# Kernel tuning notes

Hardware: AMD Instinct MI355X
Metric: run time of the kernel (lower is better)

The kernel has to match this reference:

```python
import jax, jax.numpy as jnp
import numpy as np

N = 100000
E = 3200000
IN_DIM = 256
HID = 128
OUT_DIM = 64


def setup_inputs() -> dict:
    key = jax.random.key(0)
    ks = jax.random.split(key, 8)
    features = jax.random.normal(ks[0], (N, IN_DIM), dtype=jnp.float32)
    edge_row = jax.random.randint(ks[1], (E,), 0, N, dtype=jnp.int32)
    edge_col = jax.random.randint(ks[2], (E,), 0, N, dtype=jnp.int32)
    edge_val = jax.random.uniform(ks[3], (E,), dtype=jnp.float32)
    W1 = jax.random.normal(ks[4], (IN_DIM, HID), dtype=jnp.float32) * (1.0 / np.sqrt(IN_DIM))
    b1 = jnp.zeros((HID,), dtype=jnp.float32)
    W2 = jax.random.normal(ks[5], (HID, OUT_DIM), dtype=jnp.float32) * (1.0 / np.sqrt(HID))
    b2 = jnp.zeros((OUT_DIM,), dtype=jnp.float32)
    return {"features": features, "edge_row": edge_row, "edge_col": edge_col,
            "edge_val": edge_val, "W1": W1, "b1": b1, "W2": W2, "b2": b2}


def reference(features, edge_row, edge_col, edge_val, W1, b1, W2, b2):
    # fc1: [N, IN_DIM] @ [IN_DIM, HID] + b1
    h = features @ W1 + b1                                   # [N, HID]
    # spmm(A, h): for each edge (r, c, v): out[r] += v * h[c]
    msgs = edge_val[:, None] * h[edge_col]                    # [E, HID] gather
    h = jax.ops.segment_sum(msgs, edge_row, num_segments=N)   # [N, HID] scatter-add
    h = jax.nn.relu(h)
    h = h @ W2 + b2                                           # [N, OUT_DIM]
    return jax.nn.log_softmax(h, axis=1)
```

## Files before the change

### kernel.cpp

```cpp
#include <hip/hip_runtime.h>
#include <math.h>

constexpr int IN_DIM  = 256;
constexpr int HID     = 128;
constexpr int OUT_DIM = 64;

constexpr int BROWS   = 128;
constexpr int NBUCK   = 782;
constexpr int CAP     = 4608;
constexpr int CAP2    = 5504;
constexpr int CHUNK2  = 2048;
constexpr int GC_STRIDE = 16;

typedef short  bf16x8 __attribute__((ext_vector_type(8)));
typedef float  f32x4  __attribute__((ext_vector_type(4)));
typedef float  f32x2  __attribute__((ext_vector_type(2)));
typedef int    i32x4  __attribute__((ext_vector_type(4)));

__device__ __forceinline__ unsigned short f2bf(float x) {
    union { float f; unsigned u; } v; v.f = x;
    unsigned r = v.u + 0x7FFF + ((v.u >> 16) & 1);
    return (unsigned short)(r >> 16);
}

__global__ __launch_bounds__(256) void wt_kernel(const float* __restrict__ W1,
                                                 const float* __restrict__ W2,
                                                 unsigned short* __restrict__ W1T,
                                                 unsigned short* __restrict__ W2T)
{
    int idx = blockIdx.x * 256 + threadIdx.x;
    if (idx < IN_DIM * HID) {
        int k = idx >> 7;
        int n = idx & 127;
        W1T[n * IN_DIM + k] = f2bf(W1[idx]);
    } else {
        int j = idx - IN_DIM * HID;
        int k = j >> 6;
        int n = j & 63;
        W2T[n * HID + k] = f2bf(W2[j]);
    }
}

__global__ __launch_bounds__(256) void fc1_bin_fused(
        const float* __restrict__ feat,
        const unsigned short* __restrict__ W1T,
        const float* __restrict__ b1,
        unsigned short* __restrict__ h1b, int N,
        const int* __restrict__ erow,
        const int* __restrict__ ecol,
        const float* __restrict__ eval,
        int* __restrict__ gCursor,
        int2* __restrict__ binned, int E)
{
    __shared__ int sCnt[NBUCK];
    __shared__ int sBase[NBUCK];

    const int nfc1 = (N + 63) >> 6;
    const int nbin = (E + CHUNK2 - 1) / CHUNK2;
    const int nInter = 2 * min(nfc1, nbin);
    const int b = blockIdx.x;

    bool isBin;
    int  id;
    if (b < nInter) { isBin = (b & 1); id = b >> 1; }
    else            { isBin = (nbin > nfc1); id = min(nfc1, nbin) + (b - nInter); }

    const int t = threadIdx.x;

    if (!isBin) {
        const int lane = t & 63;
        const int w    = t >> 6;
        const int quad = lane >> 4;
        const int ln15 = lane & 15;
        const int row0 = id * 64;

        int arow = row0 + w * 16 + ln15;
        if (arow >= N) arow = N - 1;
        const float* aptr = feat + (size_t)arow * IN_DIM + quad * 8;

        f32x4 acc[8];
#pragma unroll
        for (int i = 0; i < 8; ++i) acc[i] = (f32x4){0.f, 0.f, 0.f, 0.f};

#pragma unroll
        for (int ks = 0; ks < 8; ++ks) {
            float4 a0 = *(const float4*)(aptr + ks * 32);
            float4 a1 = *(const float4*)(aptr + ks * 32 + 4);
            bf16x8 afrag;
            afrag[0] = (short)f2bf(a0.x); afrag[1] = (short)f2bf(a0.y);
            afrag[2] = (short)f2bf(a0.z); afrag[3] = (short)f2bf(a0.w);
            afrag[4] = (short)f2bf(a1.x); afrag[5] = (short)f2bf(a1.y);
            afrag[6] = (short)f2bf(a1.z); afrag[7] = (short)f2bf(a1.w);
#pragma unroll
            for (int nt = 0; nt < 8; ++nt) {
                bf16x8 bfrag = *(const bf16x8*)&W1T[(size_t)(nt * 16 + ln15) * IN_DIM + ks * 32 + quad * 8];
                acc[nt] = __builtin_amdgcn_mfma_f32_16x16x32_bf16(afrag, bfrag, acc[nt], 0, 0, 0);
            }
        }

#pragma unroll
        for (int nt = 0; nt < 8; ++nt) {
            int col = nt * 16 + ln15;
            float bias = b1[col];
#pragma unroll
            for (int r = 0; r < 4; ++r) {
                int grow = row0 + w * 16 + quad * 4 + r;
                if (grow < N)
                    h1b[(size_t)grow * HID + col] = f2bf(acc[nt][r] + bias);
            }
        }
    } else {
        const int e0   = id * CHUNK2;
        const int eEnd = min(e0 + CHUNK2, E);

        for (int i = t; i < NBUCK; i += 256) sCnt[i] = 0;
        __syncthreads();

        for (int e = e0 + t; e < eEnd; e += 256)
            atomicAdd(&sCnt[erow[e] >> 7], 1);
        __syncthreads();

        for (int i = t; i < NBUCK; i += 256) {
            int c = sCnt[i];
            sBase[i] = c ? atomicAdd(&gCursor[i * GC_STRIDE], c) : 0;
            sCnt[i] = 0;
        }
        __syncthreads();

        for (int e = e0 + t; e < eEnd; e += 256) {
            int   r = erow[e];
            int   c = ecol[e];
            float v = eval[e];
            int   bk = r >> 7;
            int off = sBase[bk] + atomicAdd(&sCnt[bk], 1);
            if (off < CAP)
                binned[(size_t)bk * CAP + off] = make_int2((c << 8) | ((r & 127) << 25),
                                                           __float_as_int(v));
        }
    }
}

__global__ __launch_bounds__(256) void sort_bucket4(const int* __restrict__ gCursor,
                                                    const int2* __restrict__ binned,
                                                    int2* __restrict__ edges2,
                                                    int2* __restrict__ rowIdx, int N)
{
    __shared__ int2 sE[CAP];
    __shared__ int sHist[BROWS];
    __shared__ int sStart[BROWS + 1];
    __shared__ int sCur[BROWS];
    const int t  = threadIdx.x;
    const int b  = blockIdx.x;
    const int nE = min(gCursor[b * GC_STRIDE], CAP);
    const size_t baseIn  = (size_t)b * CAP;
    const size_t baseOut = (size_t)b * CAP2;

    if (t < BROWS) sHist[t] = 0;
    __syncthreads();

    for (int i = t; i < nE; i += 256) {
        int2 p = binned[baseIn + i];
        sE[i] = p;
        atomicAdd(&sHist[(unsigned)p.x >> 25], 1);
    }
    __syncthreads();

    if (t < BROWS) sStart[t + 1] = (sHist[t] + 7) & ~7;
    if (t == 0) sStart[0] = 0;
    __syncthreads();
    for (int o = 1; o < BROWS; o <<= 1) {
        int v = 0;
        if (t < BROWS) {
            v = sStart[t + 1];
            if (t >= o) v += sStart[t + 1 - o];
        }
        __syncthreads();
        if (t < BROWS) sStart[t + 1] = v;
        __syncthreads();
    }
    if (t < BROWS) sCur[t] = sStart[t];
    __syncthreads();

    for (int i = t; i < nE; i += 256) {
        int2 p = sE[i];
        int rl = (unsigned)p.x >> 25;
        int pos = atomicAdd(&sCur[rl], 1);
        edges2[baseOut + pos] = p;
    }

    if (t < BROWS) {
        int h  = sHist[t];
        int ph = (h + 7) & ~7;
        size_t p0 = baseOut + sStart[t];
        for (int k = h; k < ph; ++k)
            edges2[p0 + k] = make_int2(0, 0);
        int rr = b * BROWS + t;
        if (rr < N)
            rowIdx[rr] = make_int2((int)p0, (int)(p0 + ph));
    }
}

__global__ __launch_bounds__(256) void spmm_kernel(const int2* __restrict__ rowIdx,
                                                   const int2* __restrict__ edges2,
                                                   const unsigned short* __restrict__ h1b,
                                                   unsigned* __restrict__ h2b, int N)
{
    const int lane  = threadIdx.x & 63;
    const int lane4 = lane * 4;
    const int r     = (blockIdx.x * blockDim.x + threadIdx.x) >> 6;
    if (r >= N) return;
    const char* h1base = (const char*)h1b;

    const int2 se = rowIdx[r];
    int j = se.x;
    const int jend = se.y;
    f32x2 acc = (f32x2){0.f, 0.f};

    for (; j + 16 <= jend; j += 16) {
        i32x4 q[8];
#pragma unroll
        for (int u = 0; u < 8; ++u)
            q[u] = __builtin_nontemporal_load((const i32x4*)&edges2[j + u * 2]);
        unsigned g[16];
#pragma unroll
        for (int u = 0; u < 8; ++u) {
            g[2 * u]     = *(const unsigned*)(h1base + (q[u].x & 0x01FFFFFF) + lane4);
            g[2 * u + 1] = *(const unsigned*)(h1base + (q[u].z & 0x01FFFFFF) + lane4);
        }
#pragma unroll
        for (int u = 0; u < 8; ++u) {
            f32x2 h0 = (f32x2){__uint_as_float(g[2 * u] << 16),
                               __uint_as_float(g[2 * u] & 0xFFFF0000u)};
            f32x2 h1 = (f32x2){__uint_as_float(g[2 * u + 1] << 16),
                               __uint_as_float(g[2 * u + 1] & 0xFFFF0000u)};
            acc += h0 * __int_as_float(q[u].y);
            acc += h1 * __int_as_float(q[u].w);
        }
    }
    if (j < jend) {
        i32x4 q[4];
#pragma unroll
        for (int u = 0; u < 4; ++u)
            q[u] = __builtin_nontemporal_load((const i32x4*)&edges2[j + u * 2]);
        unsigned g[8];
#pragma unroll
        for (int u = 0; u < 4; ++u) {
            g[2 * u]     = *(const unsigned*)(h1base + (q[u].x & 0x01FFFFFF) + lane4);
            g[2 * u + 1] = *(const unsigned*)(h1base + (q[u].z & 0x01FFFFFF) + lane4);
        }
#pragma unroll
        for (int u = 0; u < 4; ++u) {
            f32x2 h0 = (f32x2){__uint_as_float(g[2 * u] << 16),
                               __uint_as_float(g[2 * u] & 0xFFFF0000u)};
            f32x2 h1 = (f32x2){__uint_as_float(g[2 * u + 1] << 16),
                               __uint_as_float(g[2 * u + 1] & 0xFFFF0000u)};
            acc += h0 * __int_as_float(q[u].y);
            acc += h1 * __int_as_float(q[u].w);
        }
    }

    float ax = fmaxf(acc.x, 0.f), ay = fmaxf(acc.y, 0.f);
    h2b[(size_t)r * 64 + lane] = (unsigned)f2bf(ax) | ((unsigned)f2bf(ay) << 16);
}

__global__ __launch_bounds__(256) void fc2_mfma(const unsigned short* __restrict__ h2b,
                                                const unsigned short* __restrict__ W2T,
                                                const float* __restrict__ b2,
                                                float* __restrict__ out, int N)
{
    const int t    = threadIdx.x;
    const int lane = t & 63;
    const int w    = t >> 6;
    const int quad = lane >> 4;
    const int ln15 = lane & 15;
    const int row0 = blockIdx.x * 64;

    int arow = row0 + w * 16 + ln15;
    if (arow >= N) arow = N - 1;

    f32x4 acc[4];
#pragma unroll
    for (int i = 0; i < 4; ++i) acc[i] = (f32x4){0.f, 0.f, 0.f, 0.f};

#pragma unroll
    for (int ks = 0; ks < 4; ++ks) {
        bf16x8 afrag = *(const bf16x8*)&h2b[(size_t)arow * HID + ks * 32 + quad * 8];
#pragma unroll
        for (int nt = 0; nt < 4; ++nt) {
            bf16x8 bfrag = *(const bf16x8*)&W2T[(size_t)(nt * 16 + ln15) * HID + ks * 32 + quad * 8];
            acc[nt] = __builtin_amdgcn_mfma_f32_16x16x32_bf16(afrag, bfrag, acc[nt], 0, 0, 0);
        }
    }

    float bias[4];
#pragma unroll
    for (int nt = 0; nt < 4; ++nt) bias[nt] = b2[nt * 16 + ln15];

#pragma unroll
    for (int r = 0; r < 4; ++r) {
        float v[4];
#pragma unroll
        for (int nt = 0; nt < 4; ++nt) v[nt] = acc[nt][r] + bias[nt];

        float m = fmaxf(fmaxf(v[0], v[1]), fmaxf(v[2], v[3]));
#pragma unroll
        for (int o = 1; o < 16; o <<= 1) m = fmaxf(m, __shfl_xor(m, o));
        float s = __expf(v[0] - m) + __expf(v[1] - m) +
                  __expf(v[2] - m) + __expf(v[3] - m);
#pragma unroll
        for (int o = 1; o < 16; o <<= 1) s += __shfl_xor(s, o);
        float ls = __logf(s);

        int grow = row0 + w * 16 + quad * 4 + r;
        if (grow < N) {
#pragma unroll
            for (int nt = 0; nt < 4; ++nt)
                out[(size_t)grow * OUT_DIM + nt * 16 + ln15] = v[nt] - m - ls;
        }
    }
}

extern "C" void kernel_launch(void* const* d_in, const int* in_sizes, int n_in,
                              void* d_out, int out_size, void* d_ws, size_t ws_size,
                              hipStream_t stream) {
    const float* feat = (const float*)d_in[0];
    const int*   erow = (const int*)d_in[1];
    const int*   ecol = (const int*)d_in[2];
    const float* eval = (const float*)d_in[3];
    const float* W1   = (const float*)d_in[4];
    const float* b1   = (const float*)d_in[5];
    const float* W2   = (const float*)d_in[6];
    const float* b2   = (const float*)d_in[7];
    float*       out  = (float*)d_out;

    const int N = in_sizes[0] / IN_DIM;
    const int E = in_sizes[1];

    unsigned short* h1b    = (unsigned short*)d_ws;
    unsigned short* h2b    = h1b + (size_t)N * HID;
    int2*           binned = (int2*)(h2b + (size_t)N * HID);
    int2*           edges2 = binned + (size_t)NBUCK * CAP;
    int2*           rowIdx = edges2 + (size_t)NBUCK * CAP2;
    unsigned short* W1T    = (unsigned short*)(rowIdx + N);
    unsigned short* W2T    = W1T + IN_DIM * HID;
    int*            gCursor= (int*)(W2T + HID * OUT_DIM);

    hipMemsetAsync(gCursor, 0, NBUCK * GC_STRIDE * sizeof(int), stream);

    wt_kernel<<<(IN_DIM * HID + HID * OUT_DIM) / 256, 256, 0, stream>>>(W1, W2, W1T, W2T);

    const int nfc1 = (N + 63) / 64;
    const int nbin = (E + CHUNK2 - 1) / CHUNK2;
    fc1_bin_fused<<<nfc1 + nbin, 256, 0, stream>>>(feat, W1T, b1, h1b, N,
                                                   erow, ecol, eval,
                                                   gCursor, binned, E);

    sort_bucket4<<<NBUCK, 256, 0, stream>>>(gCursor, binned, edges2, rowIdx, N);

    const int nblk = (N + 3) / 4;
    spmm_kernel<<<nblk, 256, 0, stream>>>(rowIdx, edges2, h1b,
                                          (unsigned*)h2b, N);
    fc2_mfma<<<(N + 63) / 64, 256, 0, stream>>>(h2b, W2T, b2, out, N);
}
```

Baseline: 477.7 us.

## Fuse SpMM and fc2/log-softmax into one kernel using LDS-staged fp32 W2

Merges the SpMM kernel and the MFMA fc2 kernel into a single 512-thread kernel. Each wave aggregates one row, applies ReLU and writes it to LDS. It then computes the 64 fc2 outputs with scalar FMAs against W2, which each block copies into LDS as fp32, and finishes with the log-softmax via wave shuffles. This removes the bf16 h2 intermediate write and read and one kernel launch, and drops the W2 transpose. In exchange, every block reloads the 32KB W2 from cache, needs about 36KB of LDS, waits on a barrier before starting its gathers, and replaces the MFMA matmul with plain FMAs.

```diff
diff --git a/kernel.cpp b/kernel.cpp
--- a/kernel.cpp
+++ b/kernel.cpp
@@ -24,21 +24,12 @@
 }
 
 __global__ __launch_bounds__(256) void wt_kernel(const float* __restrict__ W1,
-                                                 const float* __restrict__ W2,
-                                                 unsigned short* __restrict__ W1T,
-                                                 unsigned short* __restrict__ W2T)
+                                                 unsigned short* __restrict__ W1T)
 {
     int idx = blockIdx.x * 256 + threadIdx.x;
-    if (idx < IN_DIM * HID) {
-        int k = idx >> 7;
-        int n = idx & 127;
-        W1T[n * IN_DIM + k] = f2bf(W1[idx]);
-    } else {
-        int j = idx - IN_DIM * HID;
-        int k = j >> 6;
-        int n = j & 63;
-        W2T[n * HID + k] = f2bf(W2[j]);
-    }
+    int k = idx >> 7;
+    int n = idx & 127;
+    W1T[n * IN_DIM + k] = f2bf(W1[idx]);
 }
 
 __global__ __launch_bounds__(256) void fc1_bin_fused(
@@ -200,123 +191,102 @@
     }
 }
 
-__global__ __launch_bounds__(256) void spmm_kernel(const int2* __restrict__ rowIdx,
-                                                   const int2* __restrict__ edges2,
-                                                   const unsigned short* __restrict__ h1b,
-                                                   unsigned* __restrict__ h2b, int N)
-{
-    const int lane  = threadIdx.x & 63;
-    const int lane4 = lane * 4;
-    const int r     = (blockIdx.x * blockDim.x + threadIdx.x) >> 6;
-    if (r >= N) return;
-    const char* h1base = (const char*)h1b;
-
-    const int2 se = rowIdx[r];
-    int j = se.x;
-    const int jend = se.y;
-    f32x2 acc = (f32x2){0.f, 0.f};
-
-    for (; j + 16 <= jend; j += 16) {
-        i32x4 q[8];
-#pragma unroll
-        for (int u = 0; u < 8; ++u)
-            q[u] = __builtin_nontemporal_load((const i32x4*)&edges2[j + u * 2]);
-        unsigned g[16];
-#pragma unroll
-        for (int u = 0; u < 8; ++u) {
-            g[2 * u]     = *(const unsigned*)(h1base + (q[u].x & 0x01FFFFFF) + lane4);
-            g[2 * u + 1] = *(const unsigned*)(h1base + (q[u].z & 0x01FFFFFF) + lane4);
-        }
-#pragma unroll
-        for (int u = 0; u < 8; ++u) {
-            f32x2 h0 = (f32x2){__uint_as_float(g[2 * u] << 16),
-                               __uint_as_float(g[2 * u] & 0xFFFF0000u)};
-            f32x2 h1 = (f32x2){__uint_as_float(g[2 * u + 1] << 16),
-                               __uint_as_float(g[2 * u + 1] & 0xFFFF0000u)};
-            acc += h0 * __int_as_float(q[u].y);
-            acc += h1 * __int_as_float(q[u].w);
-        }
-    }
-    if (j < jend) {
-        i32x4 q[4];
-#pragma unroll
-        for (int u = 0; u < 4; ++u)
-            q[u] = __builtin_nontemporal_load((const i32x4*)&edges2[j + u * 2]);
-        unsigned g[8];
-#pragma unroll
-        for (int u = 0; u < 4; ++u) {
-            g[2 * u]     = *(const unsigned*)(h1base + (q[u].x & 0x01FFFFFF) + lane4);
-            g[2 * u + 1] = *(const unsigned*)(h1base + (q[u].z & 0x01FFFFFF) + lane4);
-        }
-#pragma unroll
-        for (int u = 0; u < 4; ++u) {
-            f32x2 h0 = (f32x2){__uint_as_float(g[2 * u] << 16),
-                               __uint_as_float(g[2 * u] & 0xFFFF0000u)};
-            f32x2 h1 = (f32x2){__uint_as_float(g[2 * u + 1] << 16),
-                               __uint_as_float(g[2 * u + 1] & 0xFFFF0000u)};
-            acc += h0 * __int_as_float(q[u].y);
-            acc += h1 * __int_as_float(q[u].w);
-        }
-    }
-
-    float ax = fmaxf(acc.x, 0.f), ay = fmaxf(acc.y, 0.f);
-    h2b[(size_t)r * 64 + lane] = (unsigned)f2bf(ax) | ((unsigned)f2bf(ay) << 16);
-}
-
-__global__ __launch_bounds__(256) void fc2_mfma(const unsigned short* __restrict__ h2b,
-                                                const unsigned short* __restrict__ W2T,
+__global__ __launch_bounds__(512) void spmm_fc2(const int2* __restrict__ rowIdx,
+                                                const int2* __restrict__ edges2,
+                                                const unsigned short* __restrict__ h1b,
+                                                const float* __restrict__ W2,
                                                 const float* __restrict__ b2,
                                                 float* __restrict__ out, int N)
 {
+    __shared__ __align__(16) float sW2[HID * OUT_DIM];
+    __shared__ float sH2[8][HID];
     const int t    = threadIdx.x;
     const int lane = t & 63;
-    const int w    = t >> 6;
-    const int quad = lane >> 4;
-    const int ln15 = lane & 15;
-    const int row0 = blockIdx.x * 64;
-
-    int arow = row0 + w * 16 + ln15;
-    if (arow >= N) arow = N - 1;
-
-    f32x4 acc[4];
-#pragma unroll
-    for (int i = 0; i < 4; ++i) acc[i] = (f32x4){0.f, 0.f, 0.f, 0.f};
-
-#pragma unroll
-    for (int ks = 0; ks < 4; ++ks) {
-        bf16x8 afrag = *(const bf16x8*)&h2b[(size_t)arow * HID + ks * 32 + quad * 8];
-#pragma unroll
-        for (int nt = 0; nt < 4; ++nt) {
-            bf16x8 bfrag = *(const bf16x8*)&W2T[(size_t)(nt * 16 + ln15) * HID + ks * 32 + quad * 8];
-            acc[nt] = __builtin_amdgcn_mfma_f32_16x16x32_bf16(afrag, bfrag, acc[nt], 0, 0, 0);
-        }
-    }
-
-    float bias[4];
-#pragma unroll
-    for (int nt = 0; nt < 4; ++nt) bias[nt] = b2[nt * 16 + ln15];
-
-#pragma unroll
-    for (int r = 0; r < 4; ++r) {
-        float v[4];
-#pragma unroll
-        for (int nt = 0; nt < 4; ++nt) v[nt] = acc[nt][r] + bias[nt];
-
-        float m = fmaxf(fmaxf(v[0], v[1]), fmaxf(v[2], v[3]));
-#pragma unroll
-        for (int o = 1; o < 16; o <<= 1) m = fmaxf(m, __shfl_xor(m, o));
-        float s = __expf(v[0] - m) + __expf(v[1] - m) +
-                  __expf(v[2] - m) + __expf(v[3] - m);
-#pragma unroll
-        for (int o = 1; o < 16; o <<= 1) s += __shfl_xor(s, o);
-        float ls = __logf(s);
-
-        int grow = row0 + w * 16 + quad * 4 + r;
-        if (grow < N) {
-#pragma unroll
-            for (int nt = 0; nt < 4; ++nt)
-                out[(size_t)grow * OUT_DIM + nt * 16 + ln15] = v[nt] - m - ls;
-        }
+    const int wv   = t >> 6;
+
+#pragma unroll
+    for (int i = 0; i < 4; ++i) {
+        int f = i * 512 + t;
+        *(float4*)&sW2[f * 4] = *(const float4*)&W2[f * 4];
+    }
+    __syncthreads();
+
+    const int r = blockIdx.x * 8 + wv;
+    float ax = 0.f, ay = 0.f;
+
+    if (r < N) {
+        const int lane4 = lane * 4;
+        const char* h1base = (const char*)h1b;
+        const int2 se = rowIdx[r];
+        int j = se.x;
+        const int jend = se.y;
+        f32x2 acc = (f32x2){0.f, 0.f};
+
+        for (; j + 16 <= jend; j += 16) {
+            i32x4 q[8];
+#pragma unroll
+            for (int u = 0; u < 8; ++u)
+                q[u] = __builtin_nontemporal_load((const i32x4*)&edges2[j + u * 2]);
+            unsigned g[16];
+#pragma unroll
+            for (int u = 0; u < 8; ++u) {
+                g[2 * u]     = *(const unsigned*)(h1base + (q[u].x & 0x01FFFFFF) + lane4);
+                g[2 * u + 1] = *(const unsigned*)(h1base + (q[u].z & 0x01FFFFFF) + lane4);
+            }
+#pragma unroll
+            for (int u = 0; u < 8; ++u) {
+                f32x2 h0 = (f32x2){__uint_as_float(g[2 * u] << 16),
+                                   __uint_as_float(g[2 * u] & 0xFFFF0000u)};
+                f32x2 h1 = (f32x2){__uint_as_float(g[2 * u + 1] << 16),
+                                   __uint_as_float(g[2 * u + 1] & 0xFFFF0000u)};
+                acc += h0 * __int_as_float(q[u].y);
+                acc += h1 * __int_as_float(q[u].w);
+            }
+        }
+        if (j < jend) {
+            i32x4 q[4];
+#pragma unroll
+            for (int u = 0; u < 4; ++u)
+                q[u] = __builtin_nontemporal_load((const i32x4*)&edges2[j + u * 2]);
+            unsigned g[8];
+#pragma unroll
+            for (int u = 0; u < 4; ++u) {
+                g[2 * u]     = *(const unsigned*)(h1base + (q[u].x & 0x01FFFFFF) + lane4);
+                g[2 * u + 1] = *(const unsigned*)(h1base + (q[u].z & 0x01FFFFFF) + lane4);
+            }
+#pragma unroll
+            for (int u = 0; u < 4; ++u) {
+                f32x2 h0 = (f32x2){__uint_as_float(g[2 * u] << 16),
+                                   __uint_as_float(g[2 * u] & 0xFFFF0000u)};
+                f32x2 h1 = (f32x2){__uint_as_float(g[2 * u + 1] << 16),
+                                   __uint_as_float(g[2 * u + 1] & 0xFFFF0000u)};
+                acc += h0 * __int_as_float(q[u].y);
+                acc += h1 * __int_as_float(q[u].w);
+            }
+        }
+        ax = fmaxf(acc.x, 0.f);
+        ay = fmaxf(acc.y, 0.f);
+    }
+
+    sH2[wv][lane * 2]     = ax;
+    sH2[wv][lane * 2 + 1] = ay;
+
+    if (r < N) {
+        float acc = b2[lane];
+        const float* w2l = &sW2[lane];
+#pragma unroll 8
+        for (int k = 0; k < HID; ++k)
+            acc = fmaf(sH2[wv][k], w2l[k * OUT_DIM], acc);
+
+        float m = acc;
+#pragma unroll
+        for (int o = 1; o < 64; o <<= 1) m = fmaxf(m, __shfl_xor(m, o));
+        float e = __expf(acc - m);
+        float s = e;
+#pragma unroll
+        for (int o = 1; o < 64; o <<= 1) s += __shfl_xor(s, o);
+
+        out[(size_t)r * OUT_DIM + lane] = acc - m - __logf(s);
     }
 }
 
@@ -337,17 +307,15 @@
     const int E = in_sizes[1];
 
     unsigned short* h1b    = (unsigned short*)d_ws;
-    unsigned short* h2b    = h1b + (size_t)N * HID;
-    int2*           binned = (int2*)(h2b + (size_t)N * HID);
+    int2*           binned = (int2*)(h1b + (size_t)N * HID);
     int2*           edges2 = binned + (size_t)NBUCK * CAP;
     int2*           rowIdx = edges2 + (size_t)NBUCK * CAP2;
     unsigned short* W1T    = (unsigned short*)(rowIdx + N);
-    unsigned short* W2T    = W1T + IN_DIM * HID;
-    int*            gCursor= (int*)(W2T + HID * OUT_DIM);
+    int*            gCursor= (int*)(W1T + IN_DIM * HID);
 
     hipMemsetAsync(gCursor, 0, NBUCK * GC_STRIDE * sizeof(int), stream);
 
-    wt_kernel<<<(IN_DIM * HID + HID * OUT_DIM) / 256, 256, 0, stream>>>(W1, W2, W1T, W2T);
+    wt_kernel<<<(IN_DIM * HID) / 256, 256, 0, stream>>>(W1, W1T);
 
     const int nfc1 = (N + 63) / 64;
     const int nbin = (E + CHUNK2 - 1) / CHUNK2;
@@ -357,8 +325,6 @@
 
     sort_bucket4<<<NBUCK, 256, 0, stream>>>(gCursor, binned, edges2, rowIdx, N);
 
-    const int nblk = (N + 3) / 4;
-    spmm_kernel<<<nblk, 256, 0, stream>>>(rowIdx, edges2, h1b,
-                                          (unsigned*)h2b, N);
-    fc2_mfma<<<(N + 63) / 64, 256, 0, stream>>>(h2b, W2T, b2, out, N);
-}
+    const int nblk = (N + 7) / 8;
+    spmm_fc2<<<nblk, 512, 0, stream>>>(rowIdx, edges2, h1b, W2, b2, out, N);
+}
```

Measured after the change: 464.6 us. 1.03x faster.
